# Optimization experiments

Measured on AMD Instinct MI355X. Metric: run time of the kernel, lower is better.

Reference implementation:

```python
import jax, jax.numpy as jnp
import numpy as np

LN_EPS = 1e-5


def _expert(x, w1, b1, gamma, beta, w2, b2):
    # Linear(input_dim,24) -> LayerNorm(24) -> SiLU -> (Dropout=id in eval) -> Linear(24,16) -> SiLU
    h = x @ w1 + b1                                  # [B,24]
    mu = jnp.mean(h, axis=-1, keepdims=True)
    var = jnp.mean(jnp.square(h - mu), axis=-1, keepdims=True)
    h = (h - mu) * jax.lax.rsqrt(var + LN_EPS) * gamma + beta
    h = jax.nn.silu(h)
    return jax.nn.silu(h @ w2 + b2)                  # [B,16]


def setup_inputs() -> dict:
    key = jax.random.key(0)
    ks = jax.random.split(key, 16)
    D = 16  # input_dim
    s = 0.1
    inp = {
        "x": jax.random.normal(ks[0], (2097152, D), dtype=jnp.float32),
        # gate: Linear(D,8) -> Tanh -> Linear(8,2)
        "gw1": jax.random.normal(ks[1], (D, 8), dtype=jnp.float32) * s,
        "gb1": jnp.zeros((8,), jnp.float32),
        "gw2": jax.random.normal(ks[2], (8, 2), dtype=jnp.float32) * s,
        "gb2": jnp.zeros((2,), jnp.float32),
        # expert1
        "e1w1": jax.random.normal(ks[3], (D, 24), dtype=jnp.float32) * s,
        "e1b1": jnp.zeros((24,), jnp.float32),
        "e1g": jnp.ones((24,), jnp.float32),
        "e1bn": jnp.zeros((24,), jnp.float32),
        "e1w2": jax.random.normal(ks[4], (24, 16), dtype=jnp.float32) * s,
        "e1b2": jnp.zeros((16,), jnp.float32),
        # expert2
        "e2w1": jax.random.normal(ks[5], (D, 24), dtype=jnp.float32) * s,
        "e2b1": jnp.zeros((24,), jnp.float32),
        "e2g": jnp.ones((24,), jnp.float32),
        "e2bn": jnp.zeros((24,), jnp.float32),
        "e2w2": jax.random.normal(ks[6], (24, 16), dtype=jnp.float32) * s,
        "e2b2": jnp.zeros((16,), jnp.float32),
        # trunk: Linear(16,16) -> SiLU -> (Dropout=id)
        "tw": jax.random.normal(ks[7], (16, 16), dtype=jnp.float32) * s,
        "tb": jnp.zeros((16,), jnp.float32),
        # heads
        "sw": jax.random.normal(ks[8], (16, 1), dtype=jnp.float32) * s,
        "sb": jnp.zeros((1,), jnp.float32),
        "hw": jax.random.normal(ks[9], (16, 2), dtype=jnp.float32) * s,
        "hb": jnp.zeros((2,), jnp.float32),
    }
    return inp


def reference(x, gw1, gb1, gw2, gb2,
              e1w1, e1b1, e1g, e1bn, e1w2, e1b2,
              e2w1, e2b1, e2g, e2bn, e2w2, e2b2,
              tw, tb, sw, sb, hw, hb):
    gate_logits = jnp.tanh(x @ gw1 + gb1) @ gw2 + gb2        # [B,2]
    gate_w = jax.nn.softmax(gate_logits, axis=-1)
    h1 = _expert(x, e1w1, e1b1, e1g, e1bn, e1w2, e1b2)       # [B,16]
    h2 = _expert(x, e2w1, e2b1, e2g, e2bn, e2w2, e2b2)       # [B,16]
    h = gate_w[:, :1] * h1 + gate_w[:, 1:] * h2              # [B,16]
    h = jax.nn.silu(h @ tw + tb)                             # trunk (dropout=id)
    strain = h @ sw + sb                                     # [B,1]
    hs = h @ hw + hb                                         # [B,2]
    tensile_raw = hs[:, :1]
    gap = jax.nn.softplus(hs[:, 1:])
    yield_strength = tensile_raw - gap
    return jnp.concatenate([strain, tensile_raw, yield_strength], axis=-1)  # [B,3]
```

## Files before the change

### kernel.cpp

```cpp
#include <hip/hip_runtime.h>

#define LN_EPS 1e-5f

typedef _Float16 f16x4 __attribute__((ext_vector_type(4)));
typedef float f32x4 __attribute__((ext_vector_type(4)));
typedef unsigned int u32;
typedef u32 u32x2 __attribute__((ext_vector_type(2)));

#if defined(__HIP_DEVICE_COMPILE__)
#  if __has_builtin(__builtin_amdgcn_mfma_f32_16x16x16f16)
#    define MFMA16(a, b, c) __builtin_amdgcn_mfma_f32_16x16x16f16(a, b, c, 0, 0, 0)
#  elif __has_builtin(__builtin_amdgcn_mfma_f32_16x16x16_f16)
#    define MFMA16(a, b, c) __builtin_amdgcn_mfma_f32_16x16x16_f16(a, b, c, 0, 0, 0)
#  else
#    error "no 16x16x16 f16 mfma builtin on device"
#  endif
#else
#  define MFMA16(a, b, c) (c)
#endif

__device__ __forceinline__ float fast_rcp(float x) { return __builtin_amdgcn_rcpf(x); }

__device__ __forceinline__ u32 pk2(float a, float b) {
    return __builtin_bit_cast(u32, __builtin_amdgcn_cvt_pkrtz(a, b));
}
__device__ __forceinline__ f16x4 mk4(float a, float b, float c, float d) {
    u32x2 t = {pk2(a, b), pk2(c, d)};
    return __builtin_bit_cast(f16x4, t);
}

__device__ __forceinline__ void silu_pair(float a0, float a1, float& s0, float& s1) {
    float t0 = __expf(fminf(-a0, 80.0f));
    float t1 = __expf(fminf(-a1, 80.0f));
    float d0 = 1.0f + t0, d1 = 1.0f + t1;
    float rp = fast_rcp(d0 * d1);
    s0 = a0 * (d1 * rp);
    s1 = a1 * (d0 * rp);
}
__device__ __forceinline__ void tanh_pair(float x0, float x1, float& r0, float& r1) {
    float t0 = __expf(fminf(-2.0f * x0, 80.0f));
    float t1 = __expf(fminf(-2.0f * x1, 80.0f));
    float d0 = 1.0f + t0, d1 = 1.0f + t1;
    float rp = fast_rcp(d0 * d1);
    r0 = fmaf(2.0f, d1 * rp, -1.0f);
    r1 = fmaf(2.0f, d0 * rp, -1.0f);
}
__device__ __forceinline__ float softplus_f(float x) {
    float e = __expf(-fabsf(x));
    return fmaxf(x, 0.0f) + __logf(1.0f + e);
}


__device__ __forceinline__ float aval(int m, int row, int k,
                                      const float* gw1, const float* gw2,
                                      const float* e1w1, const float* e1w2,
                                      const float* e2w1, const float* e2w2,
                                      const float* tw, const float* sw, const float* hw) {
    switch (m) {
        case 0:  return (row < 8) ? gw1[k * 8 + row] : 0.0f;
        case 1:  return (row < 2 && k < 8) ? gw2[k * 2 + row] : 0.0f;
        case 2:  return e1w1[k * 24 + row];
        case 3:  return (row < 8) ? e1w1[k * 24 + 16 + row] : 0.0f;
        case 4:  return e1w2[k * 16 + row];
        case 5:  return (k < 8) ? e1w2[(16 + k) * 16 + row] : 0.0f;
        case 6:  return e2w1[k * 24 + row];
        case 7:  return (row < 8) ? e2w1[k * 24 + 16 + row] : 0.0f;
        case 8:  return e2w2[k * 16 + row];
        case 9:  return (k < 8) ? e2w2[(16 + k) * 16 + row] : 0.0f;
        case 10: return tw[k * 16 + row];
        default:
            if (row == 0) return sw[k];
            if (row == 1) return hw[2 * k + 0];
            if (row == 2) return hw[2 * k + 1];
            return 0.0f;
    }
}

__device__ __forceinline__ float bval(int bf, int row,
                                      const float* gb1, const float* gb2,
                                      const float* e1b1, const float* e1b2,
                                      const float* e2b1, const float* e2b2,
                                      const float* tb, const float* sb, const float* hb) {
    switch (bf) {
        case 0:  return (row < 8) ? gb1[row] : 0.0f;
        case 1:  return (row < 2) ? gb2[row] : 0.0f;
        case 2:  return e1b1[row];
        case 3:  return (row < 8) ? e1b1[16 + row] : 0.0f;
        case 4:  return e1b2[row];
        case 5:  return e2b1[row];
        case 6:  return (row < 8) ? e2b1[16 + row] : 0.0f;
        case 7:  return e2b2[row];
        case 8:  return tb[row];
        default:
            if (row == 0) return sb[0];
            if (row == 1) return hb[0];
            if (row == 2) return hb[1];
            return 0.0f;
    }
}

__global__ void pack_frags(const float* __restrict__ gw1, const float* __restrict__ gb1,
                           const float* __restrict__ gw2, const float* __restrict__ gb2,
                           const float* __restrict__ e1w1, const float* __restrict__ e1b1,
                           const float* __restrict__ e1g, const float* __restrict__ e1bn,
                           const float* __restrict__ e1w2, const float* __restrict__ e1b2,
                           const float* __restrict__ e2w1, const float* __restrict__ e2b1,
                           const float* __restrict__ e2g, const float* __restrict__ e2bn,
                           const float* __restrict__ e2w2, const float* __restrict__ e2b2,
                           const float* __restrict__ tw, const float* __restrict__ tb,
                           const float* __restrict__ sw, const float* __restrict__ sb,
                           const float* __restrict__ hw, const float* __restrict__ hb,
                           u32* __restrict__ ws) {
    int t = blockIdx.x * blockDim.x + threadIdx.x;
    if (t < 1536) {
        int m = t >> 7, rem = t & 127, lane = rem >> 1, d = rem & 1;
        int row = lane & 15, k0 = (lane >> 4) * 4 + 2 * d;
        float v0 = aval(m, row, k0,     gw1, gw2, e1w1, e1w2, e2w1, e2w2, tw, sw, hw);
        float v1 = aval(m, row, k0 + 1, gw1, gw2, e1w1, e1w2, e2w1, e2w2, tw, sw, hw);
        ws[t] = pk2(v0, v1);
    } else if (t < 4096) {
        int f = t - 1536;
        int bf = f >> 8, rem = f & 255, lane = rem >> 2, r = rem & 3;
        int row = (lane >> 4) * 4 + r;
        float v = bval(bf, row, gb1, gb2, e1b1, e1b2, e2b1, e2b2, tb, sb, hb);
        ((float*)ws)[t] = v;
    } else if (t < 6144) {
        int f = t - 4096;
        int nf = f >> 8, rem = f & 255, lane = rem >> 2, r = rem & 3;
        int e = nf >> 2, w = nf & 3, g_ = lane >> 4;
        const float* ge = e ? e2g : e1g;
        const float* bne = e ? e2bn : e1bn;
        float v;
        if (w < 2) {
            int feat = g_ * 4 + r;
            v = (w == 0) ? ge[feat] : bne[feat];
        } else {
            int feat = 16 + g_ * 4 + r;
            v = (g_ < 2) ? ((w == 2) ? ge[feat] : bne[feat]) : 0.0f;
        }
        ((float*)ws)[t] = v;
    }
}

template <bool FIRST>
__device__ __forceinline__ void expert_mfma(f16x4 A1a, f16x4 A1b, f16x4 A2a, f16x4 A2b,
                                            f32x4 b1a, f32x4 b1b, f32x4 b2,
                                            f32x4 gc1, f32x4 bc1, f32x4 gc2, f32x4 bc2,
                                            f16x4 Bx, float scale, f32x4& h) {
    f32x4 C1 = MFMA16(A1a, Bx, b1a);
    f32x4 C2 = MFMA16(A1b, Bx, b1b);
    float E = (C1[0] + C1[1]) + (C1[2] + C1[3]) + (C2[0] + C2[1]) + (C2[2] + C2[3]);
    float E2 = 0.0f;
#pragma unroll
    for (int i = 0; i < 4; ++i) E2 = fmaf(C1[i], C1[i], E2);
#pragma unroll
    for (int i = 0; i < 4; ++i) E2 = fmaf(C2[i], C2[i], E2);
    E  += __shfl_xor(E, 16);  E  += __shfl_xor(E, 32);
    E2 += __shfl_xor(E2, 16); E2 += __shfl_xor(E2, 32);
    float mu = E * (1.0f / 24.0f);
    float var = fmaf(E2, 1.0f / 24.0f, -mu * mu);
    float rstd = rsqrtf(var + LN_EPS);
    float n[8], sv[8];
#pragma unroll
    for (int i = 0; i < 4; ++i) n[i]     = fmaf((C1[i] - mu) * rstd, gc1[i], bc1[i]);
#pragma unroll
    for (int i = 0; i < 4; ++i) n[4 + i] = fmaf((C2[i] - mu) * rstd, gc2[i], bc2[i]);
    silu_pair(n[0], n[1], sv[0], sv[1]);
    silu_pair(n[2], n[3], sv[2], sv[3]);
    silu_pair(n[4], n[5], sv[4], sv[5]);
    silu_pair(n[6], n[7], sv[6], sv[7]);
    f16x4 B1 = mk4(sv[0], sv[1], sv[2], sv[3]);
    f16x4 B2 = mk4(sv[4], sv[5], sv[6], sv[7]);
    f32x4 O = MFMA16(A2a, B1, b2);
    O = MFMA16(A2b, B2, O);
    float so0, so1, so2, so3;
    silu_pair(O[0], O[1], so0, so1);
    silu_pair(O[2], O[3], so2, so3);
    if (FIRST) {
        h[0] = scale * so0; h[1] = scale * so1; h[2] = scale * so2; h[3] = scale * so3;
    } else {
        h[0] = fmaf(scale, so0, h[0]); h[1] = fmaf(scale, so1, h[1]);
        h[2] = fmaf(scale, so2, h[2]); h[3] = fmaf(scale, so3, h[3]);
    }
}

__global__ __launch_bounds__(256) void moe_mfma_kernel(const float* __restrict__ x,
                                                       const u32* __restrict__ ws,
                                                       float* __restrict__ out, int nrows) {
    const f16x4* Afr = (const f16x4*)ws;
    const float* wsf = (const float*)ws;
    const f32x4* Bfr = (const f32x4*)(wsf + 1536);
    const f32x4* Nfr = (const f32x4*)(wsf + 4096);

    int lane = threadIdx.x & 63;
    int g = lane >> 4, s = lane & 15;
    int wid = (blockIdx.x * blockDim.x + threadIdx.x) >> 6;
    int nw = (gridDim.x * blockDim.x) >> 6;

    f16x4 Ag1 = Afr[0 * 64 + lane], Ag2 = Afr[1 * 64 + lane];
    f16x4 A1a = Afr[2 * 64 + lane], A1b = Afr[3 * 64 + lane];
    f16x4 A2a = Afr[4 * 64 + lane], A2b = Afr[5 * 64 + lane];
    f16x4 A3a = Afr[6 * 64 + lane], A3b = Afr[7 * 64 + lane];
    f16x4 A4a = Afr[8 * 64 + lane], A4b = Afr[9 * 64 + lane];
    f16x4 Atr = Afr[10 * 64 + lane], Ahd = Afr[11 * 64 + lane];
    f32x4 Bg1 = Bfr[0 * 64 + lane], Bg2 = Bfr[1 * 64 + lane];
    f32x4 Be1a = Bfr[2 * 64 + lane], Be1b = Bfr[3 * 64 + lane], Be1o = Bfr[4 * 64 + lane];
    f32x4 Be2a = Bfr[5 * 64 + lane], Be2b = Bfr[6 * 64 + lane], Be2o = Bfr[7 * 64 + lane];
    f32x4 Btr = Bfr[8 * 64 + lane], Bhd = Bfr[9 * 64 + lane];
    f32x4 G1c1 = Nfr[0 * 64 + lane], B1c1 = Nfr[1 * 64 + lane];
    f32x4 G1c2 = Nfr[2 * 64 + lane], B1c2 = Nfr[3 * 64 + lane];
    f32x4 G2c1 = Nfr[4 * 64 + lane], B2c1 = Nfr[5 * 64 + lane];
    f32x4 G2c2 = Nfr[6 * 64 + lane], B2c2 = Nfr[7 * 64 + lane];

    int ntiles = (nrows + 15) >> 4;
    for (int tile = wid; tile < ntiles; tile += nw) {
        int r0 = tile * 16 + s;
        int rc = r0 < nrows ? r0 : nrows - 1;
        const f32x4 xv = *(const f32x4*)(x + (size_t)rc * 16 + g * 4);
        f16x4 Bx = mk4(xv[0], xv[1], xv[2], xv[3]);

        f32x4 Cg = MFMA16(Ag1, Bx, Bg1);
        float t0, t1, t2, t3;
        tanh_pair(Cg[0], Cg[1], t0, t1);
        tanh_pair(Cg[2], Cg[3], t2, t3);
        f16x4 Bt = mk4(t0, t1, t2, t3);
        f32x4 Cl = MFMA16(Ag2, Bt, Bg2);
        float l0 = __shfl(Cl[0], s, 64);
        float l1 = __shfl(Cl[1], s, 64);
        float w0 = fast_rcp(1.0f + __expf(l1 - l0));
        float w1 = 1.0f - w0;

        f32x4 h;
        expert_mfma<true >(A1a, A1b, A2a, A2b, Be1a, Be1b, Be1o, G1c1, B1c1, G1c2, B1c2, Bx, w0, h);
        expert_mfma<false>(A3a, A3b, A4a, A4b, Be2a, Be2b, Be2o, G2c1, B2c1, G2c2, B2c2, Bx, w1, h);

        f16x4 Bh = mk4(h[0], h[1], h[2], h[3]);
        f32x4 Ct = MFMA16(Atr, Bh, Btr);
        float u0, u1, u2, u3;
        silu_pair(Ct[0], Ct[1], u0, u1);
        silu_pair(Ct[2], Ct[3], u2, u3);
        f16x4 Bu = mk4(u0, u1, u2, u3);

        f32x4 Ch = MFMA16(Ahd, Bu, Bhd);
        if (g == 0 && r0 < nrows) {
            float strain = Ch[0];
            float tens = Ch[1];
            float yld = tens - softplus_f(Ch[2]);
            size_t o = (size_t)r0 * 3;
            out[o + 0] = strain;
            out[o + 1] = tens;
            out[o + 2] = yld;
        }
    }
}

extern "C" void kernel_launch(void* const* d_in, const int* in_sizes, int n_in,
                              void* d_out, int out_size, void* d_ws, size_t ws_size,
                              hipStream_t stream) {
    const float* x    = (const float*)d_in[0];
    const float* gw1  = (const float*)d_in[1];
    const float* gb1  = (const float*)d_in[2];
    const float* gw2  = (const float*)d_in[3];
    const float* gb2  = (const float*)d_in[4];
    const float* e1w1 = (const float*)d_in[5];
    const float* e1b1 = (const float*)d_in[6];
    const float* e1g  = (const float*)d_in[7];
    const float* e1bn = (const float*)d_in[8];
    const float* e1w2 = (const float*)d_in[9];
    const float* e1b2 = (const float*)d_in[10];
    const float* e2w1 = (const float*)d_in[11];
    const float* e2b1 = (const float*)d_in[12];
    const float* e2g  = (const float*)d_in[13];
    const float* e2bn = (const float*)d_in[14];
    const float* e2w2 = (const float*)d_in[15];
    const float* e2b2 = (const float*)d_in[16];
    const float* tw   = (const float*)d_in[17];
    const float* tb   = (const float*)d_in[18];
    const float* sw   = (const float*)d_in[19];
    const float* sb   = (const float*)d_in[20];
    const float* hw   = (const float*)d_in[21];
    const float* hb   = (const float*)d_in[22];
    float* out = (float*)d_out;
    u32* ws = (u32*)d_ws;

    pack_frags<<<24, 256, 0, stream>>>(gw1, gb1, gw2, gb2,
                                       e1w1, e1b1, e1g, e1bn, e1w2, e1b2,
                                       e2w1, e2b1, e2g, e2bn, e2w2, e2b2,
                                       tw, tb, sw, sb, hw, hb, ws);

    int nrows = in_sizes[0] / 16;
    moe_mfma_kernel<<<2048, 256, 0, stream>>>(x, ws, out, nrows);
}
```

Before: 122.1 us.

## Prefetch next x tile, batch SiLU/tanh reciprocals, replicate gate weights to drop shuffles

Loads the next tile's input rows into registers before computing the current tile, so global-load latency overlaps the MFMA and activation chain. SiLU and tanh now share one reciprocal across four values instead of two, with the exponent clamp lowered from 80 to 20 so the product of four denominators stays within float range. Gate weights and biases are replicated across every group of four output rows, so each lane already holds both gate logits and the two cross-lane shuffles go away. The prefetch adds register pressure, and the shared reciprocal with the tighter clamp may cost a little accuracy.

```diff
diff --git a/kernel.cpp b/kernel.cpp
--- a/kernel.cpp
+++ b/kernel.cpp
@@ -29,22 +29,38 @@
     return __builtin_bit_cast(f16x4, t);
 }
 
-__device__ __forceinline__ void silu_pair(float a0, float a1, float& s0, float& s1) {
-    float t0 = __expf(fminf(-a0, 80.0f));
-    float t1 = __expf(fminf(-a1, 80.0f));
-    float d0 = 1.0f + t0, d1 = 1.0f + t1;
-    float rp = fast_rcp(d0 * d1);
-    s0 = a0 * (d1 * rp);
-    s1 = a1 * (d0 * rp);
-}
-__device__ __forceinline__ void tanh_pair(float x0, float x1, float& r0, float& r1) {
-    float t0 = __expf(fminf(-2.0f * x0, 80.0f));
-    float t1 = __expf(fminf(-2.0f * x1, 80.0f));
-    float d0 = 1.0f + t0, d1 = 1.0f + t1;
-    float rp = fast_rcp(d0 * d1);
-    r0 = fmaf(2.0f, d1 * rp, -1.0f);
-    r1 = fmaf(2.0f, d0 * rp, -1.0f);
-}
+__device__ __forceinline__ void silu_quad(float a0, float a1, float a2, float a3,
+                                          float& s0, float& s1, float& s2, float& s3) {
+    float t0 = __expf(fminf(-a0, 20.0f));
+    float t1 = __expf(fminf(-a1, 20.0f));
+    float t2 = __expf(fminf(-a2, 20.0f));
+    float t3 = __expf(fminf(-a3, 20.0f));
+    float d0 = 1.0f + t0, d1 = 1.0f + t1, d2 = 1.0f + t2, d3 = 1.0f + t3;
+    float d01 = d0 * d1, d23 = d2 * d3;
+    float rp = fast_rcp(d01 * d23);
+    float q01 = d23 * rp, q23 = d01 * rp;
+    s0 = a0 * (d1 * q01);
+    s1 = a1 * (d0 * q01);
+    s2 = a2 * (d3 * q23);
+    s3 = a3 * (d2 * q23);
+}
+
+__device__ __forceinline__ void tanh_quad(float x0, float x1, float x2, float x3,
+                                          float& r0, float& r1, float& r2, float& r3) {
+    float t0 = __expf(fminf(-2.0f * x0, 20.0f));
+    float t1 = __expf(fminf(-2.0f * x1, 20.0f));
+    float t2 = __expf(fminf(-2.0f * x2, 20.0f));
+    float t3 = __expf(fminf(-2.0f * x3, 20.0f));
+    float d0 = 1.0f + t0, d1 = 1.0f + t1, d2 = 1.0f + t2, d3 = 1.0f + t3;
+    float d01 = d0 * d1, d23 = d2 * d3;
+    float rp = fast_rcp(d01 * d23);
+    float q01 = d23 * rp, q23 = d01 * rp;
+    r0 = fmaf(2.0f, d1 * q01, -1.0f);
+    r1 = fmaf(2.0f, d0 * q01, -1.0f);
+    r2 = fmaf(2.0f, d3 * q23, -1.0f);
+    r3 = fmaf(2.0f, d2 * q23, -1.0f);
+}
+
 __device__ __forceinline__ float softplus_f(float x) {
     float e = __expf(-fabsf(x));
     return fmaxf(x, 0.0f) + __logf(1.0f + e);
@@ -58,7 +74,7 @@
                                       const float* tw, const float* sw, const float* hw) {
     switch (m) {
         case 0:  return (row < 8) ? gw1[k * 8 + row] : 0.0f;
-        case 1:  return (row < 2 && k < 8) ? gw2[k * 2 + row] : 0.0f;
+        case 1:  return ((row & 3) < 2 && k < 8) ? gw2[k * 2 + (row & 3)] : 0.0f;
         case 2:  return e1w1[k * 24 + row];
         case 3:  return (row < 8) ? e1w1[k * 24 + 16 + row] : 0.0f;
         case 4:  return e1w2[k * 16 + row];
@@ -83,7 +99,7 @@
                                       const float* tb, const float* sb, const float* hb) {
     switch (bf) {
         case 0:  return (row < 8) ? gb1[row] : 0.0f;
-        case 1:  return (row < 2) ? gb2[row] : 0.0f;
+        case 1:  return ((row & 3) < 2) ? gb2[row & 3] : 0.0f;
         case 2:  return e1b1[row];
         case 3:  return (row < 8) ? e1b1[16 + row] : 0.0f;
         case 4:  return e1b2[row];
@@ -165,17 +181,14 @@
     for (int i = 0; i < 4; ++i) n[i]     = fmaf((C1[i] - mu) * rstd, gc1[i], bc1[i]);
 #pragma unroll
     for (int i = 0; i < 4; ++i) n[4 + i] = fmaf((C2[i] - mu) * rstd, gc2[i], bc2[i]);
-    silu_pair(n[0], n[1], sv[0], sv[1]);
-    silu_pair(n[2], n[3], sv[2], sv[3]);
-    silu_pair(n[4], n[5], sv[4], sv[5]);
-    silu_pair(n[6], n[7], sv[6], sv[7]);
+    silu_quad(n[0], n[1], n[2], n[3], sv[0], sv[1], sv[2], sv[3]);
+    silu_quad(n[4], n[5], n[6], n[7], sv[4], sv[5], sv[6], sv[7]);
     f16x4 B1 = mk4(sv[0], sv[1], sv[2], sv[3]);
     f16x4 B2 = mk4(sv[4], sv[5], sv[6], sv[7]);
     f32x4 O = MFMA16(A2a, B1, b2);
     O = MFMA16(A2b, B2, O);
     float so0, so1, so2, so3;
-    silu_pair(O[0], O[1], so0, so1);
-    silu_pair(O[2], O[3], so2, so3);
+    silu_quad(O[0], O[1], O[2], O[3], so0, so1, so2, so3);
     if (FIRST) {
         h[0] = scale * so0; h[1] = scale * so1; h[2] = scale * so2; h[3] = scale * so3;
     } else {
@@ -213,21 +226,33 @@
     f32x4 G2c2 = Nfr[6 * 64 + lane], B2c2 = Nfr[7 * 64 + lane];
 
     int ntiles = (nrows + 15) >> 4;
+    int nclamp = nrows - 1;
+
+    f32x4 xv;
+    {
+        int r0 = wid * 16 + s;
+        int rc = r0 < nrows ? r0 : nclamp;
+        xv = *(const f32x4*)(x + (size_t)rc * 16 + g * 4);
+    }
+
     for (int tile = wid; tile < ntiles; tile += nw) {
+        f32x4 xnext;
+        {
+            int tn = tile + nw;
+            int r0n = (tn < ntiles ? tn : tile) * 16 + s;
+            int rcn = r0n < nrows ? r0n : nclamp;
+            xnext = *(const f32x4*)(x + (size_t)rcn * 16 + g * 4);
+        }
+
         int r0 = tile * 16 + s;
-        int rc = r0 < nrows ? r0 : nrows - 1;
-        const f32x4 xv = *(const f32x4*)(x + (size_t)rc * 16 + g * 4);
         f16x4 Bx = mk4(xv[0], xv[1], xv[2], xv[3]);
 
         f32x4 Cg = MFMA16(Ag1, Bx, Bg1);
         float t0, t1, t2, t3;
-        tanh_pair(Cg[0], Cg[1], t0, t1);
-        tanh_pair(Cg[2], Cg[3], t2, t3);
+        tanh_quad(Cg[0], Cg[1], Cg[2], Cg[3], t0, t1, t2, t3);
         f16x4 Bt = mk4(t0, t1, t2, t3);
         f32x4 Cl = MFMA16(Ag2, Bt, Bg2);
-        float l0 = __shfl(Cl[0], s, 64);
-        float l1 = __shfl(Cl[1], s, 64);
-        float w0 = fast_rcp(1.0f + __expf(l1 - l0));
+        float w0 = fast_rcp(1.0f + __expf(Cl[1] - Cl[0]));
         float w1 = 1.0f - w0;
 
         f32x4 h;
@@ -237,8 +262,7 @@
         f16x4 Bh = mk4(h[0], h[1], h[2], h[3]);
         f32x4 Ct = MFMA16(Atr, Bh, Btr);
         float u0, u1, u2, u3;
-        silu_pair(Ct[0], Ct[1], u0, u1);
-        silu_pair(Ct[2], Ct[3], u2, u3);
+        silu_quad(Ct[0], Ct[1], Ct[2], Ct[3], u0, u1, u2, u3);
         f16x4 Bu = mk4(u0, u1, u2, u3);
 
         f32x4 Ch = MFMA16(Ahd, Bu, Bhd);
@@ -251,6 +275,8 @@
             out[o + 1] = tens;
             out[o + 2] = yld;
         }
+
+        xv = xnext;
     }
 }
 
```

New measurement: 123.9 us. No clear change (+1.5%).
